# Kernel tuning notes

Measured on AMD Instinct MI355X. Metric: run time of the kernel, lower is better.

## Reference

```python
import jax, jax.numpy as jnp
import numpy as np
from jax import lax

N, C, H, W = 16, 512, 64, 64
INTER, HEADS, GROUPS, K = 512, 64, 8, 7
HEAD_DIM = INTER // HEADS


def setup_inputs() -> dict:
    key = jax.random.key(0)
    ks = jax.random.split(key, 12)
    s = 0.02
    return {
        "x": jax.random.normal(ks[0], (N, C, H, W), jnp.float32),
        "conv_w": jax.random.normal(ks[1], (INTER, C // GROUPS, K, K), jnp.float32) * s,
        "conv_b": jax.random.normal(ks[2], (INTER,), jnp.float32) * s,
        "ln_g": jnp.ones((INTER,), jnp.float32),
        "ln_b": jnp.zeros((INTER,), jnp.float32),
        "qw": jax.random.normal(ks[3], (INTER, INTER), jnp.float32) * s,
        "qb": jax.random.normal(ks[4], (INTER,), jnp.float32) * s,
        "kw": jax.random.normal(ks[5], (INTER, INTER), jnp.float32) * s,
        "kb": jax.random.normal(ks[6], (INTER,), jnp.float32) * s,
        "vw": jax.random.normal(ks[7], (INTER, INTER), jnp.float32) * s,
        "vb": jax.random.normal(ks[8], (INTER,), jnp.float32) * s,
        "pw": jax.random.normal(ks[9], (C, INTER), jnp.float32) * s,
        "pb": jax.random.normal(ks[10], (C,), jnp.float32) * s,
        "beta": jax.random.normal(ks[11], (1,), jnp.float32),
    }


def reference(x, conv_w, conv_b, ln_g, ln_b, qw, qb, kw, kb, vw, vb, pw, pb, beta):
    n, c, h, w = x.shape
    hw = h * w
    pad = (K - 1) // 2
    # grouped conv, NCHW
    xc = lax.conv_general_dilated(
        x, conv_w, window_strides=(1, 1), padding=[(pad, pad), (pad, pad)],
        dimension_numbers=("NCHW", "OIHW", "NCHW"), feature_group_count=GROUPS)
    xc = xc + conv_b[None, :, None, None]
    xc = xc.reshape(n, INTER, hw).transpose(0, 2, 1)  # [N, HW, INTER]
    # LayerNorm over channel dim
    mu = jnp.mean(xc, axis=-1, keepdims=True)
    var = jnp.mean(jnp.square(xc - mu), axis=-1, keepdims=True)
    xn = (xc - mu) * lax.rsqrt(var + 1e-5) * ln_g + ln_b
    # projections (torch Linear: y = x @ W.T + b)
    q = (xn @ qw.T + qb).reshape(n, hw, HEADS, HEAD_DIM).transpose(0, 2, 1, 3)  # [N,h,HW,d]
    k = (xn @ kw.T + kb).reshape(n, hw, HEADS, HEAD_DIM).transpose(0, 2, 3, 1)  # [N,h,d,HW]
    v = (xn @ vw.T + vb).reshape(n, hw, HEADS, HEAD_DIM).transpose(0, 2, 1, 3)  # [N,h,HW,d]
    k = jax.nn.softmax(k, axis=3)  # softmax over tokens
    corr = jnp.einsum("nhds,nhse->nhde", k, v)      # [N,h,d,d] compact context
    atten = jnp.einsum("nhsd,nhde->nhse", q, corr)  # [N,h,HW,d]
    atten = atten.transpose(0, 2, 1, 3).reshape(n, hw, INTER)
    xa = (atten @ pw.T + pb).transpose(0, 2, 1).reshape(n, c, h, w)
    return beta[0] * xa + x
```

## Files before the change

kernel.cpp:

```cpp
#include <hip/hip_runtime.h>
#include <hip/hip_bf16.h>

#define N_IMG 16
#define C_DIM 512
#define H_DIM 64
#define W_DIM 64
#define HW 4096
#define INTER 512
#define HEADS 64
#define GROUPS 8
#define KSZ 7
#define CPG 64
#define M_TOT (N_IMG * HW)

typedef short bf16x8 __attribute__((ext_vector_type(8)));
typedef short bf16x4 __attribute__((ext_vector_type(4)));
typedef float f32x4 __attribute__((ext_vector_type(4)));
typedef unsigned int u32;

__device__ __forceinline__ unsigned short f2bf(float f) {
    __hip_bfloat16 h = __float2bfloat16(f);
    return *reinterpret_cast<unsigned short*>(&h);
}
__device__ __forceinline__ float bf2f(unsigned short u) {
    u32 x = ((u32)u) << 16;
    union { u32 i; float f; } c; c.i = x; return c.f;
}
__device__ __forceinline__ void gload16(const void* g, void* l) {
    __builtin_amdgcn_global_load_lds(
        (const __attribute__((address_space(1))) u32*)g,
        (__attribute__((address_space(3))) u32*)l, 16, 0, 0);
}
__device__ __forceinline__ void raw_barrier() {
    asm volatile("" ::: "memory");
    __builtin_amdgcn_s_barrier();
    asm volatile("" ::: "memory");
}
#define WAIT_VM(N) asm volatile("s_waitcnt vmcnt(" #N ")" ::: "memory")

__global__ __launch_bounds__(256) void prep_kernel(
    const float* __restrict__ cw, const float* __restrict__ kw,
    const float* __restrict__ vw, const float* __restrict__ pw,
    const float* __restrict__ x,
    unsigned short* __restrict__ pk, unsigned short* __restrict__ kwb,
    unsigned short* __restrict__ vwb, unsigned short* __restrict__ pwb,
    float* __restrict__ crw, unsigned short* __restrict__ xb)
{
    const int b = blockIdx.x;
    const int tid = threadIdx.x;
    if (b < 6272) {
        int p = b * 256 + tid;
        int ci = p & 63;
        int co = (p >> 6) & 63;
        int r  = p >> 12;
        int dx = r % 7;
        int dyg = r / 7;
        int dy = dyg % 7;
        int g  = dyg / 7;
        float v = cw[(((size_t)(g * 64 + co)) * 64 + ci) * 49 + dy * 7 + dx];
        pk[(size_t)(g * 49 + dy * 7 + dx) * 4096 + co * 64 + (ci ^ ((co & 7) << 3))] = f2bf(v);
        return;
    }
    if (b < 8320) {
        const float* w = (b < 7296) ? kw : vw;
        unsigned short* wp = (b < 7296) ? kwb : vwb;
        int e = ((b < 7296) ? (b - 6272) : (b - 7296)) * 256 + tid;
        int j = e & 7;
        int chunk = (e >> 3) & 511;
        int kt = (e >> 12) & 15;
        int t = e >> 16;
        int col = chunk & 127, kq = chunk >> 7;
        wp[e] = f2bf(w[(size_t)(t * 128 + col) * 512 + kt * 32 + kq * 8 + j]);
        return;
    }
    if (b < 9344) {
        int i = (b - 8320) * 256 + tid;
        pwb[i] = f2bf(pw[i]);
        return;
    }
    if (b < 9632) {
        crw[(b - 9344) * 256 + tid] = 0.f;
        return;
    }
    {
        const int idx = b - 9632;
        const int n   = idx / 560;
        const int rem = idx - n * 560;
        const int g   = rem / 70;
        const int row = rem - g * 70;
        unsigned short* dst = xb + ((size_t)(n * 8 + g) * 70 + row) * 4608;

        if (row < 3 || row > 66) {
            bf16x8 z = (bf16x8){0,0,0,0,0,0,0,0};
            *(bf16x8*)&dst[tid * 8] = z;
            *(bf16x8*)&dst[(256 + tid) * 8] = z;
            if (tid < 64) *(bf16x8*)&dst[(512 + tid) * 8] = z;
            return;
        }
        const int y = row - 3;
        const int xcol = tid & 63;
        const int oct = tid >> 6;
        const int col = xcol + 3;
        const int cswz = (col & 7) << 3;
        const float* src = x + (((size_t)(n * C_DIM + g * CPG)) * H_DIM + y) * W_DIM + xcol;
#pragma unroll
        for (int h = 0; h < 2; ++h) {
            const int ci0 = oct * 16 + h * 8;
            unsigned short tmp[8];
#pragma unroll
            for (int j = 0; j < 8; ++j)
                tmp[j] = f2bf(src[(size_t)(ci0 + j) * (H_DIM * W_DIM)]);
            *(bf16x8*)&dst[col * 64 + (ci0 ^ cswz)] = *(bf16x8*)tmp;
        }
        if (tid < 64) {
            const int hc[8] = {0, 1, 2, 67, 68, 69, 70, 71};
            int c = hc[tid >> 3], o8 = (tid & 7) * 8;
            *(bf16x8*)&dst[c * 64 + (o8 ^ ((c & 7) << 3))] = (bf16x8){0,0,0,0,0,0,0,0};
        }
    }
}

__global__ __launch_bounds__(256) void conv_mfma2_kernel(
    const unsigned short* __restrict__ xb, const unsigned short* __restrict__ pk,
    const float* __restrict__ cb, unsigned short* __restrict__ xc)
{
    __shared__ __align__(16) unsigned short in_ring[4 * 72 * 64];
    __shared__ __align__(16) unsigned short w_lds[2 * 4096];

    const int bid  = blockIdx.x;
    const int wgid = (bid & 7) * 256 + (bid >> 3);
    const int g  = wgid >> 8;
    const int n  = (wgid >> 4) & 15;
    const int y0 = (wgid & 15) * 4;
    const int tid  = threadIdx.x;
    const int lane = tid & 63;
    const int wv   = tid >> 6;
    const int lx   = lane & 15;
    const int q4   = lane >> 4;
    const int koff = q4 * 8;
    const int c3   = 512 + (tid & 63);

    const unsigned short* xbase = xb + ((size_t)(n * 8 + g) * 70) * 4608;
    const unsigned short* pkg   = pk + (size_t)g * 49 * 4096;

    f32x4 acc[4][4];
#pragma unroll
    for (int i = 0; i < 4; ++i)
#pragma unroll
        for (int j = 0; j < 4; ++j) acc[i][j] = (f32x4){0.f, 0.f, 0.f, 0.f};

#pragma unroll
    for (int r = 0; r < 4; ++r) {
        const unsigned short* src = xbase + (size_t)(y0 + r) * 4608;
        gload16(src + tid * 8,         &in_ring[r * 4608 + tid * 8]);
        gload16(src + (256 + tid) * 8, &in_ring[r * 4608 + (256 + tid) * 8]);
        gload16(src + c3 * 8,          &in_ring[r * 4608 + c3 * 8]);
    }
    gload16(pkg + tid * 8,         &w_lds[tid * 8]);
    gload16(pkg + (256 + tid) * 8, &w_lds[(256 + tid) * 8]);

    for (int dy = 0; dy < 7; ++dy) {
#pragma unroll
        for (int dx = 0; dx < 7; ++dx) {
            const int t = dy * 7 + dx;
            raw_barrier();
            if (dx == 0 && dy > 0) {
                const int slot = (dy + 3) & 3;
                const unsigned short* src = xbase + (size_t)(y0 + dy + 3) * 4608;
                gload16(src + tid * 8,         &in_ring[slot * 4608 + tid * 8]);
                gload16(src + (256 + tid) * 8, &in_ring[slot * 4608 + (256 + tid) * 8]);
                gload16(src + c3 * 8,          &in_ring[slot * 4608 + c3 * 8]);
            }
            if (t < 48) {
                const unsigned short* wsrc = pkg + (size_t)(t + 1) * 4096;
                unsigned short* wdst = &w_lds[((t + 1) & 1) * 4096];
                gload16(wsrc + tid * 8,         wdst + tid * 8);
                gload16(wsrc + (256 + tid) * 8, wdst + (256 + tid) * 8);
                WAIT_VM(2);
            } else {
                WAIT_VM(0);
            }
            __builtin_amdgcn_sched_barrier(0);
            raw_barrier();
            __builtin_amdgcn_sched_barrier(0);

            __builtin_amdgcn_s_setprio(1);
            const unsigned short* wcur = &w_lds[(t & 1) * 4096];
            bf16x8 b[2][4];
#pragma unroll
            for (int kc = 0; kc < 2; ++kc)
#pragma unroll
                for (int ct = 0; ct < 4; ++ct) {
                    const int co = ct * 16 + lx;
                    b[kc][ct] = *(const bf16x8*)
                        &wcur[co * 64 + ((kc * 32 + koff) ^ ((co & 7) << 3))];
                }
            const int col  = wv * 16 + lx + dx;
            const int cswz = (col & 7) << 3;
#pragma unroll
            for (int ty = 0; ty < 4; ++ty) {
                const int slot = (dy + ty) & 3;
#pragma unroll
                for (int kc = 0; kc < 2; ++kc) {
                    bf16x8 a = *(const bf16x8*)
                        &in_ring[slot * 4608 + col * 64 + ((kc * 32 + koff) ^ cswz)];
#pragma unroll
                    for (int ct = 0; ct < 4; ++ct)
                        acc[ty][ct] = __builtin_amdgcn_mfma_f32_16x16x32_bf16(
                            a, b[kc][ct], acc[ty][ct], 0, 0, 0);
                }
            }
            __builtin_amdgcn_s_setprio(0);
        }
    }

#pragma unroll
    for (int ct = 0; ct < 4; ++ct) {
        const float bv = cb[g * 64 + ct * 16 + lx];
        const int cidx = g * 64 + ct * 16 + lx;
#pragma unroll
        for (int ty = 0; ty < 4; ++ty) {
            const int yy = y0 + ty;
#pragma unroll
            for (int r = 0; r < 4; ++r) {
                const int xx = wv * 16 + q4 * 4 + r;
                xc[((size_t)(n * HW + yy * W_DIM + xx)) * INTER + cidx]
                    = f2bf(acc[ty][ct][r] + bv);
            }
        }
    }
}

__global__ __launch_bounds__(256) void ln_kernel(
    unsigned short* __restrict__ xc, const float* __restrict__ g,
    const float* __restrict__ b)
{
    const int tid  = threadIdx.x;
    const int half = tid >> 7;
    const int l    = tid & 127;
    const size_t row = (size_t)blockIdx.x * 2 + half;

    bf16x4 u = *(const bf16x4*)(xc + row * INTER + l * 4);
    float v0 = bf2f((unsigned short)u[0]), v1 = bf2f((unsigned short)u[1]);
    float v2 = bf2f((unsigned short)u[2]), v3 = bf2f((unsigned short)u[3]);
    float s  = v0 + v1 + v2 + v3;
    float sq = v0 * v0 + v1 * v1 + v2 * v2 + v3 * v3;
#pragma unroll
    for (int off = 32; off; off >>= 1) {
        s  += __shfl_xor(s, off);
        sq += __shfl_xor(sq, off);
    }
    __shared__ float red[4][2];
    const int wid = tid >> 6;
    if ((tid & 63) == 0) { red[wid][0] = s; red[wid][1] = sq; }
    __syncthreads();
    const int w0 = half * 2;
    float S  = red[w0][0] + red[w0 + 1][0];
    float SQ = red[w0][1] + red[w0 + 1][1];
    float mu  = S * (1.f / INTER);
    float var = SQ * (1.f / INTER) - mu * mu;
    float rs  = rsqrtf(var + 1e-5f);
    float4 gg = ((const float4*)g)[l];
    float4 bb = ((const float4*)b)[l];
    bf16x4 o;
    o[0] = (short)f2bf((v0 - mu) * rs * gg.x + bb.x);
    o[1] = (short)f2bf((v1 - mu) * rs * gg.y + bb.y);
    o[2] = (short)f2bf((v2 - mu) * rs * gg.z + bb.z);
    o[3] = (short)f2bf((v3 - mu) * rs * gg.w + bb.w);
    *(bf16x4*)(xc + row * INTER + l * 4) = o;
}

__global__ __launch_bounds__(256, 2) void gemm_kv_corr_kernel(
    const unsigned short* __restrict__ A,
    const unsigned short* __restrict__ Wk, const unsigned short* __restrict__ Wv,
    const float* __restrict__ bk, const float* __restrict__ bv,
    float* __restrict__ crw, float* __restrict__ esw)
{
    __shared__ __align__(16) unsigned short pool[32768];
    unsigned short* ek_lds = pool;
    unsigned short* v_lds  = pool + 16384;

    const int tid  = threadIdx.x;
    const int lane = tid & 63;
    const int w    = tid >> 6;
    const int lx   = lane & 15;
    const int kq4  = lane >> 4;

    const int orig = blockIdx.x;
    const int wgid = (orig & 7) * 256 + (orig >> 3);
    const int m0   = (wgid >> 2) * 128;
    const int ct4  = wgid & 3;
    const int mbase = (w & 1) * 64;
    const int nbase = (w >> 1) * 64;
    const int n = m0 >> 12;

    const unsigned short* wkt = Wk + (size_t)ct4 * 65536;
    const unsigned short* wvt = Wv + (size_t)ct4 * 65536;

    f32x4 acck[4][4], accv[4][4];
#pragma unroll
    for (int i = 0; i < 4; ++i)
#pragma unroll
        for (int j = 0; j < 4; ++j) {
            acck[i][j] = (f32x4){0.f, 0.f, 0.f, 0.f};
            accv[i][j] = (f32x4){0.f, 0.f, 0.f, 0.f};
        }

#pragma unroll
    for (int it = 0; it < 2; ++it) {
        int c = it * 256 + tid;
        gload16(A + (size_t)(m0 + (c & 127)) * 512 + (c >> 7) * 8, &pool[c * 8]);
        gload16(wkt + c * 8, &pool[(1024 + c) * 8]);
        gload16(wvt + c * 8, &pool[(2048 + c) * 8]);
    }

    for (int kt = 0; kt < 16; ++kt) {
        const int b = kt & 1;
        if (kt < 15) {
            const int nb = b ^ 1;
#pragma unroll
            for (int it = 0; it < 2; ++it) {
                int c = it * 256 + tid;
                gload16(A + (size_t)(m0 + (c & 127)) * 512 + (kt + 1) * 32 + (c >> 7) * 8,
                        &pool[(nb * 512 + c) * 8]);
                gload16(wkt + (size_t)(kt + 1) * 4096 + c * 8, &pool[(1024 + nb * 512 + c) * 8]);
                gload16(wvt + (size_t)(kt + 1) * 4096 + c * 8, &pool[(2048 + nb * 512 + c) * 8]);
            }
            WAIT_VM(6);
        } else {
            WAIT_VM(0);
        }
        __builtin_amdgcn_sched_barrier(0);
        raw_barrier();
        __builtin_amdgcn_sched_barrier(0);

        __builtin_amdgcn_s_setprio(1);
        bf16x8 a[4], bkf[4], bvf[4];
#pragma unroll
        for (int i = 0; i < 4; ++i) {
            a[i]   = *(const bf16x8*)&pool[(b * 512 + kq4 * 128 + mbase + i * 16 + lx) * 8];
            bkf[i] = *(const bf16x8*)&pool[(1024 + b * 512 + kq4 * 128 + nbase + i * 16 + lx) * 8];
            bvf[i] = *(const bf16x8*)&pool[(2048 + b * 512 + kq4 * 128 + nbase + i * 16 + lx) * 8];
        }
#pragma unroll
        for (int i = 0; i < 4; ++i)
#pragma unroll
            for (int j = 0; j < 4; ++j) {
                acck[i][j] = __builtin_amdgcn_mfma_f32_16x16x32_bf16(a[i], bkf[j], acck[i][j], 0, 0, 0);
                accv[i][j] = __builtin_amdgcn_mfma_f32_16x16x32_bf16(a[i], bvf[j], accv[i][j], 0, 0, 0);
            }
        __builtin_amdgcn_s_setprio(0);
        raw_barrier();
    }

#pragma unroll
    for (int j = 0; j < 4; ++j) {
        const int colk = nbase + j * 16 + lx;
        const float bkv = bk[ct4 * 128 + colk];
        const float bvv = bv[ct4 * 128 + colk];
        const int sw = (colk & 7) << 3;
#pragma unroll
        for (int i = 0; i < 4; ++i) {
            const int t0 = mbase + i * 16 + kq4 * 4;
            const int idx = colk * 128 + (t0 ^ sw);
            bf16x4 ew, vw;
#pragma unroll
            for (int r = 0; r < 4; ++r) {
                ew[r] = (short)f2bf(__expf(acck[i][j][r] + bkv));
                vw[r] = (short)f2bf(accv[i][j][r] + bvv);
            }
            *(bf16x4*)&ek_lds[idx] = ew;
            *(bf16x4*)&v_lds[idx]  = vw;
        }
    }
    const int d = lane >> 3, e = lane & 7;
    const int hbase = (w >> 1) * 8;
#pragma unroll
    for (int h = 0; h < 8; ++h) {
        const int hb = hbase + h;
        const int ck = hb * 8 + d;
        const int ce = hb * 8 + e;
        const int swk = d << 3, swe = e << 3;
        float crh = 0.f, esh = 0.f;
#pragma unroll
        for (int tb = 0; tb < 16; ++tb) {
            const int t0 = mbase + tb * 4;
            bf16x4 ekv = *(const bf16x4*)&ek_lds[ck * 128 + (t0 ^ swk)];
            bf16x4 vvv = *(const bf16x4*)&v_lds[ce * 128 + (t0 ^ swe)];
#pragma unroll
            for (int r = 0; r < 4; ++r) {
                float ekf = bf2f((unsigned short)ekv[r]);
                crh = fmaf(ekf, bf2f((unsigned short)vvv[r]), crh);
                esh += ekf;
            }
        }
        const int nh = n * 64 + ct4 * 16 + hb;
        atomicAdd(&crw[(size_t)nh * 64 + d * 8 + e], crh);
        if (e == 0) atomicAdd(&esw[nh * 8 + d], esh);
    }
}

__global__ __launch_bounds__(256) void gcomp_kernel(
    const float* __restrict__ qw, const float* __restrict__ crw,
    const float* __restrict__ esw, unsigned short* __restrict__ G)
{
    const int h = blockIdx.x;
    const int n = blockIdx.y;
    const int tid = threadIdx.x;
    const int nh = n * 64 + h;
    __shared__ float C[64];
    if (tid < 64) C[tid] = crw[(size_t)nh * 64 + tid] / esw[nh * 8 + (tid >> 3)];
    __syncthreads();
#pragma unroll
    for (int rep = 0; rep < 2; ++rep) {
        const int k = rep * 256 + tid;
        float o[8] = {};
#pragma unroll
        for (int d = 0; d < 8; ++d) {
            float qv = qw[(size_t)(h * 8 + d) * 512 + k];
#pragma unroll
            for (int e = 0; e < 8; ++e) o[e] = fmaf(qv, C[d * 8 + e], o[e]);
        }
        bf16x8 ov;
#pragma unroll
        for (int e = 0; e < 8; ++e) ov[e] = (short)f2bf(o[e]);
        *(bf16x8*)&G[((size_t)n * 512 + k) * 512 + h * 8] = ov;
    }
}

__global__ __launch_bounds__(256) void compose_kernel(
    const unsigned short* __restrict__ Pwb, const unsigned short* __restrict__ G,
    unsigned short* __restrict__ wfp)
{
    __shared__ __align__(16) unsigned short pool[16384];
    const int tid  = threadIdx.x;
    const int lane = tid & 63;
    const int w    = tid >> 6;
    const int lx   = lane & 15;
    const int kq4  = lane >> 4;

    const int tile = blockIdx.x;
    const int n    = blockIdx.y;
    const int m0 = (tile >> 2) * 128;
    const int n0 = (tile & 3) * 128;
    const int mbase = (w & 1) * 64;
    const int nbase = (w >> 1) * 64;
    const unsigned short* Gn = G + (size_t)n * 262144;

    f32x4 acc[4][4];
#pragma unroll
    for (int i = 0; i < 4; ++i)
#pragma unroll
        for (int j = 0; j < 4; ++j) acc[i][j] = (f32x4){0.f, 0.f, 0.f, 0.f};

#pragma unroll
    for (int it = 0; it < 2; ++it) {
        int c = it * 256 + tid;
        gload16(Pwb + (size_t)(m0 + (c & 127)) * 512 + (c >> 7) * 8, &pool[c * 8]);
        gload16(Gn + (size_t)(n0 + (c & 127)) * 512 + (c >> 7) * 8, &pool[(1024 + c) * 8]);
    }
    __syncthreads();

    for (int kt = 0; kt < 16; ++kt) {
        const int b = kt & 1;
        if (kt < 15) {
            const int nb = b ^ 1;
#pragma unroll
            for (int it = 0; it < 2; ++it) {
                int c = it * 256 + tid;
                gload16(Pwb + (size_t)(m0 + (c & 127)) * 512 + (kt + 1) * 32 + (c >> 7) * 8,
                        &pool[(nb * 512 + c) * 8]);
                gload16(Gn + (size_t)(n0 + (c & 127)) * 512 + (kt + 1) * 32 + (c >> 7) * 8,
                        &pool[(1024 + nb * 512 + c) * 8]);
            }
        }
        bf16x8 a[4], bf[4];
#pragma unroll
        for (int i = 0; i < 4; ++i) {
            a[i]  = *(const bf16x8*)&pool[(b * 512 + kq4 * 128 + mbase + i * 16 + lx) * 8];
            bf[i] = *(const bf16x8*)&pool[(1024 + b * 512 + kq4 * 128 + nbase + i * 16 + lx) * 8];
        }
#pragma unroll
        for (int i = 0; i < 4; ++i)
#pragma unroll
            for (int j = 0; j < 4; ++j)
                acc[i][j] = __builtin_amdgcn_mfma_f32_16x16x32_bf16(a[i], bf[j], acc[i][j], 0, 0, 0);
        __syncthreads();
    }

    unsigned short* wfn = wfp + (size_t)n * 262144;
#pragma unroll
    for (int j = 0; j < 4; ++j) {
        const int K = n0 + nbase + j * 16 + lx;
        const int kt = K >> 5, kq = (K >> 3) & 3, jp = K & 7;
        const int ebase = (kt << 12) | (kq << 10) | jp;
#pragma unroll
        for (int i = 0; i < 4; ++i) {
            const int rowb = m0 + mbase + i * 16 + kq4 * 4;
#pragma unroll
            for (int r = 0; r < 4; ++r) {
                const int C = rowb + r;
                wfn[((C >> 7) << 16) | ebase | ((C & 127) << 3)] = f2bf(acc[i][j][r]);
            }
        }
    }
}

__global__ __launch_bounds__(256) void bias2_kernel(
    const float* __restrict__ qb, const float* __restrict__ crw,
    const float* __restrict__ esw, const float* __restrict__ pw,
    const float* __restrict__ pb, float* __restrict__ b2)
{
    const int n = blockIdx.x;
    const int tid = threadIdx.x;
    __shared__ float qbc[512];
#pragma unroll
    for (int rep = 0; rep < 2; ++rep) {
        int j = rep * 256 + tid;
        int h = j >> 3, e = j & 7;
        const int nh = n * 64 + h;
        float s = 0.f;
#pragma unroll
        for (int d = 0; d < 8; ++d)
            s += qb[h * 8 + d] * crw[(size_t)nh * 64 + d * 8 + e] / esw[nh * 8 + d];
        qbc[j] = s;
    }
    __syncthreads();
#pragma unroll
    for (int rep = 0; rep < 2; ++rep) {
        int c = rep * 256 + tid;
        const float4* pr = (const float4*)(pw + (size_t)c * 512);
        float s = pb[c];
        for (int q = 0; q < 128; ++q) {
            float4 pv = pr[q];
            s += qbc[q * 4 + 0] * pv.x + qbc[q * 4 + 1] * pv.y
               + qbc[q * 4 + 2] * pv.z + qbc[q * 4 + 3] * pv.w;
        }
        b2[n * 512 + c] = s;
    }
}

__global__ __launch_bounds__(256) void gemm_p_kernel(
    const unsigned short* __restrict__ A, const unsigned short* __restrict__ Wp,
    const float* __restrict__ bias, float* __restrict__ Y,
    const float* __restrict__ xres, const float* __restrict__ betap)
{
    __shared__ __align__(16) unsigned short pool[24576];
    const int tid  = threadIdx.x;
    const int lane = tid & 63;
    const int w    = tid >> 6;
    const int lx   = lane & 15;
    const int kq4  = lane >> 4;

    const int orig = blockIdx.x;
    const int wgid = (orig & 7) * 128 + (orig >> 3);
    const int m0 = (wgid >> 2) * 256;
    const int n0 = (wgid & 3) * 128;
    const int mbase = (w & 1) * 128;
    const int nbase = (w >> 1) * 64;
    const int nimg = m0 >> 12;

    f32x4 acc[8][4];
#pragma unroll
    for (int i = 0; i < 8; ++i)
#pragma unroll
        for (int j = 0; j < 4; ++j) acc[i][j] = (f32x4){0.f, 0.f, 0.f, 0.f};

    const unsigned short* wpt = Wp + (size_t)nimg * 262144 + (size_t)(wgid & 3) * 65536;

#pragma unroll
    for (int it = 0; it < 4; ++it) {
        int c = it * 256 + tid;
        gload16(A + (size_t)(m0 + (c & 255)) * 512 + (c >> 8) * 8, &pool[c * 8]);
    }
#pragma unroll
    for (int it = 0; it < 2; ++it) {
        int c = it * 256 + tid;
        gload16(wpt + c * 8, &pool[16384 + c * 8]);
    }

    for (int kt = 0; kt < 16; ++kt) {
        const int b = kt & 1;
        if (kt < 15) {
            const int nb = b ^ 1;
#pragma unroll
            for (int it = 0; it < 4; ++it) {
                int c = it * 256 + tid;
                gload16(A + (size_t)(m0 + (c & 255)) * 512 + (kt + 1) * 32 + (c >> 8) * 8,
                        &pool[(nb * 1024 + c) * 8]);
            }
#pragma unroll
            for (int it = 0; it < 2; ++it) {
                int c = it * 256 + tid;
                gload16(wpt + (size_t)(kt + 1) * 4096 + c * 8,
                        &pool[16384 + (nb * 512 + c) * 8]);
            }
            WAIT_VM(6);
        } else {
            WAIT_VM(0);
        }
        __builtin_amdgcn_sched_barrier(0);
        raw_barrier();
        __builtin_amdgcn_sched_barrier(0);

        __builtin_amdgcn_s_setprio(1);
        bf16x8 a[8], bf[4];
#pragma unroll
        for (int i = 0; i < 8; ++i)
            a[i] = *(const bf16x8*)&pool[(b * 1024 + kq4 * 256 + mbase + i * 16 + lx) * 8];
#pragma unroll
        for (int j = 0; j < 4; ++j)
            bf[j] = *(const bf16x8*)&pool[16384 + (b * 512 + kq4 * 128 + nbase + j * 16 + lx) * 8];
#pragma unroll
        for (int i = 0; i < 8; ++i)
#pragma unroll
            for (int j = 0; j < 4; ++j)
                acc[i][j] = __builtin_amdgcn_mfma_f32_16x16x32_bf16(a[i], bf[j], acc[i][j], 0, 0, 0);
        __builtin_amdgcn_s_setprio(0);
        raw_barrier();
    }

    const float beta = betap[0];
#pragma unroll
    for (int j = 0; j < 4; ++j) {
        const int c = n0 + nbase + j * 16 + lx;
        const float pbv = bias[nimg * 512 + c];
        const size_t cbase = ((size_t)(nimg * 512 + c)) * 4096;
#pragma unroll
        for (int i = 0; i < 8; ++i) {
            const int s = (m0 & 4095) + mbase + i * 16 + kq4 * 4;
            float4 xr = *(const float4*)(xres + cbase + s);
            float4 o;
            o.x = beta * (acc[i][j][0] + pbv) + xr.x;
            o.y = beta * (acc[i][j][1] + pbv) + xr.y;
            o.z = beta * (acc[i][j][2] + pbv) + xr.z;
            o.w = beta * (acc[i][j][3] + pbv) + xr.w;
            *(float4*)(Y + cbase + s) = o;
        }
    }
}

extern "C" void kernel_launch(void* const* d_in, const int* in_sizes, int n_in,
                              void* d_out, int out_size, void* d_ws, size_t ws_size,
                              hipStream_t stream)
{
    (void)in_sizes; (void)n_in; (void)out_size; (void)ws_size;
    const float* x   = (const float*)d_in[0];
    const float* cw  = (const float*)d_in[1];
    const float* cb  = (const float*)d_in[2];
    const float* lng = (const float*)d_in[3];
    const float* lnb = (const float*)d_in[4];
    const float* qw  = (const float*)d_in[5];
    const float* qb  = (const float*)d_in[6];
    const float* kw  = (const float*)d_in[7];
    const float* kb  = (const float*)d_in[8];
    const float* vw  = (const float*)d_in[9];
    const float* vb  = (const float*)d_in[10];
    const float* pw  = (const float*)d_in[11];
    const float* pb  = (const float*)d_in[12];
    const float* beta = (const float*)d_in[13];
    float* out = (float*)d_out;

    char* ws = (char*)d_ws;
    const size_t SZ  = (size_t)M_TOT * INTER * sizeof(float);
    const size_t HSZ = (size_t)M_TOT * INTER * 2;
    unsigned short* xc   = (unsigned short*)ws;
    unsigned short* G    = (unsigned short*)(ws + HSZ);
    unsigned short* wfp  = G + (size_t)16 * 262144;
    unsigned short* pwb  = wfp + (size_t)16 * 262144;
    float* b2            = (float*)(pwb + 262144);
    float* crw  = (float*)(ws + SZ);
    float* esw  = crw + 65536;
    unsigned short* pk  = (unsigned short*)(ws + SZ + (2 << 20));
    unsigned short* kwb = (unsigned short*)(ws + SZ + (6 << 20));
    unsigned short* vwb = kwb + 262144;
    unsigned short* xb  = vwb + 262144;

    prep_kernel<<<dim3(18592), 256, 0, stream>>>(cw, kw, vw, pw, x,
                                                 pk, kwb, vwb, pwb, crw, xb);

    conv_mfma2_kernel<<<dim3(2048), 256, 0, stream>>>(xb, pk, cb, xc);
    ln_kernel<<<dim3(M_TOT / 2), 256, 0, stream>>>(xc, lng, lnb);

    gemm_kv_corr_kernel<<<dim3(2048), 256, 0, stream>>>(xc, kwb, vwb, kb, vb, crw, esw);

    gcomp_kernel<<<dim3(64, 16), 256, 0, stream>>>(qw, crw, esw, G);
    compose_kernel<<<dim3(16, 16), 256, 0, stream>>>(pwb, G, wfp);
    bias2_kernel<<<dim3(16), 256, 0, stream>>>(qb, crw, esw, pw, pb, b2);

    gemm_p_kernel<<<dim3(1024), 256, 0, stream>>>(xc, wfp, b2, out, x, beta);
}
```

Measured before the change: 511.0 us.

## Fold LayerNorm algebraically into the conv epilogue and downstream GEMM epilogues

Removes the separate LayerNorm pass. The conv epilogue now accumulates per-token sum and sum-of-squares with atomics. The LN gain is folded into the K/V and fused projection weights, and the mean, rstd and beta terms are applied as rank-1 corrections in the GEMM epilogues using precomputed weight row sums. This avoids a full read and write of the bf16 activation tensor, at the cost of extra atomics, extra prep work, and some precision risk from running the GEMMs on un-normalized values. The s_setprio hints are also dropped.

After: 556.8 us. 9.0% more time.

```diff
diff --git a/kernel.cpp b/kernel.cpp
--- a/kernel.cpp
+++ b/kernel.cpp
@@ -41,10 +41,14 @@
 __global__ __launch_bounds__(256) void prep_kernel(
     const float* __restrict__ cw, const float* __restrict__ kw,
     const float* __restrict__ vw, const float* __restrict__ pw,
-    const float* __restrict__ x,
+    const float* __restrict__ x, const float* __restrict__ lng,
+    const float* __restrict__ lnb,
     unsigned short* __restrict__ pk, unsigned short* __restrict__ kwb,
     unsigned short* __restrict__ vwb, unsigned short* __restrict__ pwb,
-    float* __restrict__ crw, unsigned short* __restrict__ xb)
+    float* __restrict__ crw, unsigned short* __restrict__ xb,
+    float* __restrict__ sstats, float* __restrict__ s1f,
+    float* __restrict__ s1k, float* __restrict__ s2k,
+    float* __restrict__ s1v, float* __restrict__ s2v)
 {
     const int b = blockIdx.x;
     const int tid = threadIdx.x;
@@ -70,7 +74,8 @@
         int kt = (e >> 12) & 15;
         int t = e >> 16;
         int col = chunk & 127, kq = chunk >> 7;
-        wp[e] = f2bf(w[(size_t)(t * 128 + col) * 512 + kt * 32 + kq * 8 + j]);
+        int kcol = kt * 32 + kq * 8 + j;
+        wp[e] = f2bf(w[(size_t)(t * 128 + col) * 512 + kcol] * lng[kcol]);
         return;
     }
     if (b < 9344) {
@@ -82,7 +87,7 @@
         crw[(b - 9344) * 256 + tid] = 0.f;
         return;
     }
-    {
+    if (b < 18592) {
         const int idx = b - 9632;
         const int n   = idx / 560;
         const int rem = idx - n * 560;
@@ -117,12 +122,39 @@
             int c = hc[tid >> 3], o8 = (tid & 7) * 8;
             *(bf16x8*)&dst[c * 64 + (o8 ^ ((c & 7) << 3))] = (bf16x8){0,0,0,0,0,0,0,0};
         }
+        return;
+    }
+    if (b < 19104) {
+        sstats[(b - 18592) * 256 + tid] = 0.f;
+        return;
+    }
+    if (b < 19168) {
+        s1f[(b - 19104) * 256 + tid] = 0.f;
+        return;
+    }
+    {
+        const int i = b - 19168;
+        const float* w = (i < 2) ? kw : vw;
+        float* s1 = (i < 2) ? s1k : s1v;
+        float* s2 = (i < 2) ? s2k : s2v;
+        const int c = (i & 1) * 256 + tid;
+        const float4* wr = (const float4*)(w + (size_t)c * 512);
+        const float4* g4 = (const float4*)lng;
+        const float4* b4 = (const float4*)lnb;
+        float a1 = 0.f, a2 = 0.f;
+        for (int q = 0; q < 128; ++q) {
+            float4 wv4 = wr[q], gg = g4[q], bb = b4[q];
+            a1 += gg.x * wv4.x + gg.y * wv4.y + gg.z * wv4.z + gg.w * wv4.w;
+            a2 += bb.x * wv4.x + bb.y * wv4.y + bb.z * wv4.z + bb.w * wv4.w;
+        }
+        s1[c] = a1; s2[c] = a2;
     }
 }
 
 __global__ __launch_bounds__(256) void conv_mfma2_kernel(
     const unsigned short* __restrict__ xb, const unsigned short* __restrict__ pk,
-    const float* __restrict__ cb, unsigned short* __restrict__ xc)
+    const float* __restrict__ cb, unsigned short* __restrict__ xc,
+    float* __restrict__ sstats)
 {
     __shared__ __align__(16) unsigned short in_ring[4 * 72 * 64];
     __shared__ __align__(16) unsigned short w_lds[2 * 4096];
@@ -184,7 +216,6 @@
             raw_barrier();
             __builtin_amdgcn_sched_barrier(0);
 
-            __builtin_amdgcn_s_setprio(1);
             const unsigned short* wcur = &w_lds[(t & 1) * 4096];
             bf16x8 b[2][4];
 #pragma unroll
@@ -210,73 +241,52 @@
                             a, b[kc][ct], acc[ty][ct], 0, 0, 0);
                 }
             }
-            __builtin_amdgcn_s_setprio(0);
-        }
-    }
-
-#pragma unroll
-    for (int ct = 0; ct < 4; ++ct) {
-        const float bv = cb[g * 64 + ct * 16 + lx];
-        const int cidx = g * 64 + ct * 16 + lx;
-#pragma unroll
-        for (int ty = 0; ty < 4; ++ty) {
-            const int yy = y0 + ty;
-#pragma unroll
-            for (int r = 0; r < 4; ++r) {
-                const int xx = wv * 16 + q4 * 4 + r;
-                xc[((size_t)(n * HW + yy * W_DIM + xx)) * INTER + cidx]
-                    = f2bf(acc[ty][ct][r] + bv);
-            }
-        }
-    }
-}
-
-__global__ __launch_bounds__(256) void ln_kernel(
-    unsigned short* __restrict__ xc, const float* __restrict__ g,
-    const float* __restrict__ b)
-{
-    const int tid  = threadIdx.x;
-    const int half = tid >> 7;
-    const int l    = tid & 127;
-    const size_t row = (size_t)blockIdx.x * 2 + half;
-
-    bf16x4 u = *(const bf16x4*)(xc + row * INTER + l * 4);
-    float v0 = bf2f((unsigned short)u[0]), v1 = bf2f((unsigned short)u[1]);
-    float v2 = bf2f((unsigned short)u[2]), v3 = bf2f((unsigned short)u[3]);
-    float s  = v0 + v1 + v2 + v3;
-    float sq = v0 * v0 + v1 * v1 + v2 * v2 + v3 * v3;
-#pragma unroll
-    for (int off = 32; off; off >>= 1) {
-        s  += __shfl_xor(s, off);
-        sq += __shfl_xor(sq, off);
-    }
-    __shared__ float red[4][2];
-    const int wid = tid >> 6;
-    if ((tid & 63) == 0) { red[wid][0] = s; red[wid][1] = sq; }
-    __syncthreads();
-    const int w0 = half * 2;
-    float S  = red[w0][0] + red[w0 + 1][0];
-    float SQ = red[w0][1] + red[w0 + 1][1];
-    float mu  = S * (1.f / INTER);
-    float var = SQ * (1.f / INTER) - mu * mu;
-    float rs  = rsqrtf(var + 1e-5f);
-    float4 gg = ((const float4*)g)[l];
-    float4 bb = ((const float4*)b)[l];
-    bf16x4 o;
-    o[0] = (short)f2bf((v0 - mu) * rs * gg.x + bb.x);
-    o[1] = (short)f2bf((v1 - mu) * rs * gg.y + bb.y);
-    o[2] = (short)f2bf((v2 - mu) * rs * gg.z + bb.z);
-    o[3] = (short)f2bf((v3 - mu) * rs * gg.w + bb.w);
-    *(bf16x4*)(xc + row * INTER + l * 4) = o;
+        }
+    }
+
+    float bv4[4];
+#pragma unroll
+    for (int ct = 0; ct < 4; ++ct) bv4[ct] = cb[g * 64 + ct * 16 + lx];
+#pragma unroll
+    for (int ty = 0; ty < 4; ++ty) {
+        const int yy = y0 + ty;
+#pragma unroll
+        for (int r = 0; r < 4; ++r) {
+            const int xx = wv * 16 + q4 * 4 + r;
+            const int tok = n * HW + yy * W_DIM + xx;
+            float s = 0.f, sq = 0.f;
+#pragma unroll
+            for (int ct = 0; ct < 4; ++ct) {
+                const int cidx = g * 64 + ct * 16 + lx;
+                unsigned short uv = f2bf(acc[ty][ct][r] + bv4[ct]);
+                xc[(size_t)tok * INTER + cidx] = uv;
+                float fv = bf2f(uv);
+                s += fv; sq += fv * fv;
+            }
+#pragma unroll
+            for (int off = 1; off < 16; off <<= 1) {
+                s  += __shfl_xor(s, off);
+                sq += __shfl_xor(sq, off);
+            }
+            if (lx == 0) {
+                atomicAdd(&sstats[(size_t)tok * 2 + 0], s);
+                atomicAdd(&sstats[(size_t)tok * 2 + 1], sq);
+            }
+        }
+    }
 }
 
 __global__ __launch_bounds__(256, 2) void gemm_kv_corr_kernel(
     const unsigned short* __restrict__ A,
     const unsigned short* __restrict__ Wk, const unsigned short* __restrict__ Wv,
     const float* __restrict__ bk, const float* __restrict__ bv,
+    const float* __restrict__ sstats,
+    const float* __restrict__ s1k, const float* __restrict__ s2k,
+    const float* __restrict__ s1v, const float* __restrict__ s2v,
     float* __restrict__ crw, float* __restrict__ esw)
 {
     __shared__ __align__(16) unsigned short pool[32768];
+    __shared__ float mrs[256];
     unsigned short* ek_lds = pool;
     unsigned short* v_lds  = pool + 16384;
 
@@ -334,7 +344,6 @@
         raw_barrier();
         __builtin_amdgcn_sched_barrier(0);
 
-        __builtin_amdgcn_s_setprio(1);
         bf16x8 a[4], bkf[4], bvf[4];
 #pragma unroll
         for (int i = 0; i < 4; ++i) {
@@ -349,15 +358,25 @@
                 acck[i][j] = __builtin_amdgcn_mfma_f32_16x16x32_bf16(a[i], bkf[j], acck[i][j], 0, 0, 0);
                 accv[i][j] = __builtin_amdgcn_mfma_f32_16x16x32_bf16(a[i], bvf[j], accv[i][j], 0, 0, 0);
             }
-        __builtin_amdgcn_s_setprio(0);
         raw_barrier();
     }
+
+    if (tid < 128) {
+        float S  = sstats[(size_t)(m0 + tid) * 2 + 0];
+        float SQ = sstats[(size_t)(m0 + tid) * 2 + 1];
+        float mu = S * (1.f / 512.f);
+        float var = SQ * (1.f / 512.f) - mu * mu;
+        mrs[tid * 2]     = mu;
+        mrs[tid * 2 + 1] = rsqrtf(var + 1e-5f);
+    }
+    raw_barrier();
 
 #pragma unroll
     for (int j = 0; j < 4; ++j) {
         const int colk = nbase + j * 16 + lx;
-        const float bkv = bk[ct4 * 128 + colk];
-        const float bvv = bv[ct4 * 128 + colk];
+        const int cg   = ct4 * 128 + colk;
+        const float bkv = bk[cg], s1kc = s1k[cg], s2kc = s2k[cg];
+        const float bvv = bv[cg], s1vc = s1v[cg], s2vc = s2v[cg];
         const int sw = (colk & 7) << 3;
 #pragma unroll
         for (int i = 0; i < 4; ++i) {
@@ -366,8 +385,12 @@
             bf16x4 ew, vw;
 #pragma unroll
             for (int r = 0; r < 4; ++r) {
-                ew[r] = (short)f2bf(__expf(acck[i][j][r] + bkv));
-                vw[r] = (short)f2bf(accv[i][j][r] + bvv);
+                const float mu = mrs[(t0 + r) * 2];
+                const float rs = mrs[(t0 + r) * 2 + 1];
+                float kval = rs * acck[i][j][r] - rs * mu * s1kc + s2kc + bkv;
+                float vval = rs * accv[i][j][r] - rs * mu * s1vc + s2vc + bvv;
+                ew[r] = (short)f2bf(__expf(kval));
+                vw[r] = (short)f2bf(vval);
             }
             *(bf16x4*)&ek_lds[idx] = ew;
             *(bf16x4*)&v_lds[idx]  = vw;
@@ -430,7 +453,9 @@
 
 __global__ __launch_bounds__(256) void compose_kernel(
     const unsigned short* __restrict__ Pwb, const unsigned short* __restrict__ G,
-    unsigned short* __restrict__ wfp)
+    const float* __restrict__ lng, const float* __restrict__ lnb,
+    unsigned short* __restrict__ wfp, float* __restrict__ s1f,
+    float* __restrict__ s2f)
 {
     __shared__ __align__(16) unsigned short pool[16384];
     const int tid  = threadIdx.x;
@@ -494,13 +519,37 @@
         const int K = n0 + nbase + j * 16 + lx;
         const int kt = K >> 5, kq = (K >> 3) & 3, jp = K & 7;
         const int ebase = (kt << 12) | (kq << 10) | jp;
+        const float gk = lng[K];
 #pragma unroll
         for (int i = 0; i < 4; ++i) {
             const int rowb = m0 + mbase + i * 16 + kq4 * 4;
 #pragma unroll
             for (int r = 0; r < 4; ++r) {
                 const int C = rowb + r;
-                wfn[((C >> 7) << 16) | ebase | ((C & 127) << 3)] = f2bf(acc[i][j][r]);
+                wfn[((C >> 7) << 16) | ebase | ((C & 127) << 3)] = f2bf(gk * acc[i][j][r]);
+            }
+        }
+    }
+#pragma unroll
+    for (int i = 0; i < 4; ++i) {
+#pragma unroll
+        for (int r = 0; r < 4; ++r) {
+            float s1 = 0.f, s2 = 0.f;
+#pragma unroll
+            for (int j = 0; j < 4; ++j) {
+                const int K = n0 + nbase + j * 16 + lx;
+                s1 += lng[K] * acc[i][j][r];
+                s2 += lnb[K] * acc[i][j][r];
+            }
+#pragma unroll
+            for (int off = 1; off < 16; off <<= 1) {
+                s1 += __shfl_xor(s1, off);
+                s2 += __shfl_xor(s2, off);
+            }
+            if (lx == 0) {
+                const int C = m0 + mbase + i * 16 + kq4 * 4 + r;
+                atomicAdd(&s1f[n * 512 + C], s1);
+                atomicAdd(&s2f[n * 512 + C], s2);
             }
         }
     }
@@ -542,10 +591,13 @@
 
 __global__ __launch_bounds__(256) void gemm_p_kernel(
     const unsigned short* __restrict__ A, const unsigned short* __restrict__ Wp,
-    const float* __restrict__ bias, float* __restrict__ Y,
-    const float* __restrict__ xres, const float* __restrict__ betap)
+    const float* __restrict__ bias, const float* __restrict__ sstats,
+    const float* __restrict__ s1f, const float* __restrict__ s2f,
+    float* __restrict__ Y, const float* __restrict__ xres,
+    const float* __restrict__ betap)
 {
     __shared__ __align__(16) unsigned short pool[24576];
+    __shared__ float mrsP[512];
     const int tid  = threadIdx.x;
     const int lane = tid & 63;
     const int w    = tid >> 6;
@@ -603,7 +655,6 @@
         raw_barrier();
         __builtin_amdgcn_sched_barrier(0);
 
-        __builtin_amdgcn_s_setprio(1);
         bf16x8 a[8], bf[4];
 #pragma unroll
         for (int i = 0; i < 8; ++i)
@@ -616,26 +667,41 @@
 #pragma unroll
             for (int j = 0; j < 4; ++j)
                 acc[i][j] = __builtin_amdgcn_mfma_f32_16x16x32_bf16(a[i], bf[j], acc[i][j], 0, 0, 0);
-        __builtin_amdgcn_s_setprio(0);
         raw_barrier();
     }
+
+    {
+        float S  = sstats[(size_t)(m0 + tid) * 2 + 0];
+        float SQ = sstats[(size_t)(m0 + tid) * 2 + 1];
+        float mu = S * (1.f / 512.f);
+        float var = SQ * (1.f / 512.f) - mu * mu;
+        mrsP[tid * 2]     = mu;
+        mrsP[tid * 2 + 1] = rsqrtf(var + 1e-5f);
+    }
+    raw_barrier();
 
     const float beta = betap[0];
 #pragma unroll
     for (int j = 0; j < 4; ++j) {
         const int c = n0 + nbase + j * 16 + lx;
-        const float pbv = bias[nimg * 512 + c];
+        const float b2c  = bias[nimg * 512 + c];
+        const float s1fc = s1f[nimg * 512 + c];
+        const float s2fc = s2f[nimg * 512 + c];
         const size_t cbase = ((size_t)(nimg * 512 + c)) * 4096;
 #pragma unroll
         for (int i = 0; i < 8; ++i) {
-            const int s = (m0 & 4095) + mbase + i * 16 + kq4 * 4;
+            const int lt = mbase + i * 16 + kq4 * 4;
+            const int s = (m0 & 4095) + lt;
             float4 xr = *(const float4*)(xres + cbase + s);
-            float4 o;
-            o.x = beta * (acc[i][j][0] + pbv) + xr.x;
-            o.y = beta * (acc[i][j][1] + pbv) + xr.y;
-            o.z = beta * (acc[i][j][2] + pbv) + xr.z;
-            o.w = beta * (acc[i][j][3] + pbv) + xr.w;
-            *(float4*)(Y + cbase + s) = o;
+            float o[4];
+#pragma unroll
+            for (int r = 0; r < 4; ++r) {
+                const float mu = mrsP[(lt + r) * 2];
+                const float rs = mrsP[(lt + r) * 2 + 1];
+                float y = rs * acc[i][j][r] - rs * mu * s1fc + s2fc + b2c;
+                o[r] = beta * y + ((const float*)&xr)[r];
+            }
+            *(float4*)(Y + cbase + s) = *(float4*)o;
         }
     }
 }
@@ -668,7 +734,14 @@
     unsigned short* G    = (unsigned short*)(ws + HSZ);
     unsigned short* wfp  = G + (size_t)16 * 262144;
     unsigned short* pwb  = wfp + (size_t)16 * 262144;
-    float* b2            = (float*)(pwb + 262144);
+    float* b2     = (float*)(pwb + 262144);
+    float* sstats = b2 + 8192;
+    float* s1f    = sstats + 131072;
+    float* s2f    = s1f + 8192;
+    float* s1k    = s2f + 8192;
+    float* s2k    = s1k + 512;
+    float* s1v    = s2k + 512;
+    float* s2v    = s1v + 512;
     float* crw  = (float*)(ws + SZ);
     float* esw  = crw + 65536;
     unsigned short* pk  = (unsigned short*)(ws + SZ + (2 << 20));
@@ -676,17 +749,19 @@
     unsigned short* vwb = kwb + 262144;
     unsigned short* xb  = vwb + 262144;
 
-    prep_kernel<<<dim3(18592), 256, 0, stream>>>(cw, kw, vw, pw, x,
-                                                 pk, kwb, vwb, pwb, crw, xb);
-
-    conv_mfma2_kernel<<<dim3(2048), 256, 0, stream>>>(xb, pk, cb, xc);
-    ln_kernel<<<dim3(M_TOT / 2), 256, 0, stream>>>(xc, lng, lnb);
-
-    gemm_kv_corr_kernel<<<dim3(2048), 256, 0, stream>>>(xc, kwb, vwb, kb, vb, crw, esw);
+    prep_kernel<<<dim3(19172), 256, 0, stream>>>(
+        cw, kw, vw, pw, x, lng, lnb, pk, kwb, vwb, pwb, crw, xb,
+        sstats, s1f, s1k, s2k, s1v, s2v);
+
+    conv_mfma2_kernel<<<dim3(2048), 256, 0, stream>>>(xb, pk, cb, xc, sstats);
+
+    gemm_kv_corr_kernel<<<dim3(2048), 256, 0, stream>>>(
+        xc, kwb, vwb, kb, vb, sstats, s1k, s2k, s1v, s2v, crw, esw);
 
     gcomp_kernel<<<dim3(64, 16), 256, 0, stream>>>(qw, crw, esw, G);
-    compose_kernel<<<dim3(16, 16), 256, 0, stream>>>(pwb, G, wfp);
+    compose_kernel<<<dim3(16, 16), 256, 0, stream>>>(pwb, G, lng, lnb, wfp, s1f, s2f);
     bias2_kernel<<<dim3(16), 256, 0, stream>>>(qb, crw, esw, pw, pb, b2);
 
-    gemm_p_kernel<<<dim3(1024), 256, 0, stream>>>(xc, wfp, b2, out, x, beta);
-}
+    gemm_p_kernel<<<dim3(1024), 256, 0, stream>>>(
+        xc, wfp, b2, sstats, s1f, s2f, out, x, beta);
+}
```
